# Kernel optimization log

Measured on AMD Instinct MI355X. Metric: run time of the kernel, lower is better.

The kernel has to match this reference:

```python
import jax, jax.numpy as jnp
import numpy as np

NUM_HEADS = 16

def setup_inputs() -> dict:
    key = jax.random.key(0)
    k1, k2, k3 = jax.random.split(key, 3)
    D = 1024
    return {
        "hidden_states": jax.random.normal(k1, (2, 2048, D), dtype=jnp.float32),
        "c_attn_w": jax.random.normal(k2, (D, 3 * D), dtype=jnp.float32) * 0.02,
        "c_attn_b": jnp.zeros((3 * D,), dtype=jnp.float32),
        "c_proj_w": jax.random.normal(k3, (D, D), dtype=jnp.float32) * 0.02,
        "c_proj_b": jnp.zeros((D,), dtype=jnp.float32),
    }

def reference(hidden_states, c_attn_w, c_attn_b, c_proj_w, c_proj_b):
    B, S, D = hidden_states.shape
    H = NUM_HEADS
    hd = D // H
    # Conv1D: x @ W + b, then split into q, k, v
    qkv = hidden_states @ c_attn_w + c_attn_b  # [B, S, 3D]
    q, k, v = jnp.split(qkv, 3, axis=-1)
    q = q.reshape(B, S, H, hd).transpose(0, 2, 1, 3)  # [B, H, S, hd]
    k = k.reshape(B, S, H, hd).transpose(0, 2, 1, 3)
    v = v.reshape(B, S, H, hd).transpose(0, 2, 1, 3)
    # scaled QK^T
    scores = jnp.einsum("bhqd,bhkd->bhqk", q, k) / jnp.asarray(hd ** 0.5, q.dtype)
    # causal mask (tril), masked positions set to dtype min per original code
    causal = jnp.tril(jnp.ones((S, S), dtype=bool))
    mask_value = jnp.finfo(scores.dtype).min
    scores = jnp.where(causal[None, None], scores, mask_value)
    attn = jax.nn.softmax(scores, axis=-1)
    out = jnp.einsum("bhqk,bhkd->bhqd", attn, v)  # [B, H, S, hd]
    out = out.transpose(0, 2, 1, 3).reshape(B, S, D)
    out = out @ c_proj_w + c_proj_b
    return out
```

## Files before the change

kernel.cpp:

```cpp
#include <hip/hip_runtime.h>
#include <hip/hip_bf16.h>
#include <math.h>

#define B_ 2
#define S_ 2048
#define D_ 1024
#define H_ 16
#define HD 64
#define M_ (B_ * S_)
#define N_QKV (3 * D_)

typedef short short8 __attribute__((ext_vector_type(8)));
typedef float floatx4 __attribute__((ext_vector_type(4)));

static __device__ __forceinline__ unsigned short f2bf(float x) {
    __hip_bfloat16 h = __float2bfloat16(x);
    unsigned short u;
    __builtin_memcpy(&u, &h, sizeof(u));
    return u;
}
static __device__ __forceinline__ float bf2f(unsigned short b) {
    union { unsigned u; float f; } v; v.u = ((unsigned)b) << 16;
    return v.f;
}
static __device__ __forceinline__ void split2(float x, unsigned short& h, unsigned short& l) {
    h = f2bf(x);
    l = f2bf(x - bf2f(h));
}

static __device__ __forceinline__ void dma16(const void* g, void* l) {
    __builtin_amdgcn_global_load_lds(
        (const __attribute__((address_space(1))) unsigned int*)g,
        (__attribute__((address_space(3))) unsigned int*)l,
        16, 0, 0);
}

__global__ __launch_bounds__(256) void prep_A(
    const float* __restrict__ X,
    unsigned short* __restrict__ Ahi, unsigned short* __restrict__ Alo)
{
    const size_t i = ((size_t)blockIdx.x * 256 + threadIdx.x) * 8;
    float4 a = *(const float4*)(X + i);
    float4 b = *(const float4*)(X + i + 4);
    float xs[8] = {a.x, a.y, a.z, a.w, b.x, b.y, b.z, b.w};
    short8 h, l;
#pragma unroll
    for (int e = 0; e < 8; e++) {
        unsigned short hh, ll;
        split2(xs[e], hh, ll);
        h[e] = (short)hh; l[e] = (short)ll;
    }
    *(short8*)&Ahi[i] = h;
    *(short8*)&Alo[i] = l;
}

__global__ __launch_bounds__(256) void prep_wT(
    const float* __restrict__ W, int N,
    unsigned short* __restrict__ Thi, unsigned short* __restrict__ Tlo)
{
    __shared__ float Ws[64][68];
    const int t  = threadIdx.x;
    const int n0 = blockIdx.x * 64, k0 = blockIdx.y * 64;
    {
        const int kl = t >> 4, nl = (t & 15) * 4;
        const float* src = W + (size_t)(k0 + kl) * N + n0 + nl;
#pragma unroll
        for (int g = 0; g < 4; g++)
            *(float4*)&Ws[kl + g * 16][nl] = *(const float4*)(src + (size_t)g * 16 * N);
    }
    __syncthreads();
    {
        const int nl = t >> 2, ks = (t & 3) * 16;
        short8 h0, h1, l0, l1;
#pragma unroll
        for (int j = 0; j < 8; j++) {
            unsigned short hh, ll;
            split2(Ws[ks + j][nl], hh, ll);
            h0[j] = (short)hh; l0[j] = (short)ll;
        }
#pragma unroll
        for (int j = 0; j < 8; j++) {
            unsigned short hh, ll;
            split2(Ws[ks + 8 + j][nl], hh, ll);
            h1[j] = (short)hh; l1[j] = (short)ll;
        }
        unsigned short* dh = Thi + (size_t)(n0 + nl) * D_ + k0 + ks;
        unsigned short* dl = Tlo + (size_t)(n0 + nl) * D_ + k0 + ks;
        *(short8*)dh = h0; *(short8*)(dh + 8) = h1;
        *(short8*)dl = l0; *(short8*)(dl + 8) = l1;
    }
}

__global__ __launch_bounds__(256) void gemm_qkv(
    const unsigned short* __restrict__ Ahi, const unsigned short* __restrict__ Alo,
    const unsigned short* __restrict__ BThi, const unsigned short* __restrict__ BTlo,
    const float* __restrict__ bias,
    unsigned short* __restrict__ Qhi, unsigned short* __restrict__ Qlo,
    unsigned short* __restrict__ Khi, unsigned short* __restrict__ Klo,
    unsigned short* __restrict__ vThi, unsigned short* __restrict__ vTlo)
{
    __shared__ unsigned short sAh[128 * 32], sAl[128 * 32];
    __shared__ unsigned short sBh[128 * 32], sBl[128 * 32];

    const int t    = threadIdx.x;
    const int m0   = blockIdx.y * 128, n0 = blockIdx.x * 128;
    const int lane = t & 63, wave = t >> 6;
    const int lm   = lane & 15, quad = lane >> 4;
    const int wm   = (wave >> 1) * 64, wn = (wave & 1) * 64;

    const int lrow = lane >> 2, lcol = (lane & 3) * 8;
    const unsigned short* gAh = Ahi + (size_t)(m0 + wave * 32 + lrow) * D_ + lcol;
    const unsigned short* gAl = Alo + (size_t)(m0 + wave * 32 + lrow) * D_ + lcol;
    const unsigned short* gBh = BThi + (size_t)(n0 + wave * 32 + lrow) * D_ + lcol;
    const unsigned short* gBl = BTlo + (size_t)(n0 + wave * 32 + lrow) * D_ + lcol;
    const int ldst = wave * 1024 + lane * 8;

    floatx4 acc[4][4];
#pragma unroll
    for (int i = 0; i < 4; i++)
#pragma unroll
        for (int j = 0; j < 4; j++)
#pragma unroll
            for (int r = 0; r < 4; r++) acc[i][j][r] = 0.f;

    for (int k0 = 0; k0 < D_; k0 += 32) {
        __syncthreads();
        dma16(gAh + k0, &sAh[ldst]);
        dma16(gAh + (size_t)16 * D_ + k0, &sAh[ldst + 512]);
        dma16(gAl + k0, &sAl[ldst]);
        dma16(gAl + (size_t)16 * D_ + k0, &sAl[ldst + 512]);
        dma16(gBh + k0, &sBh[ldst]);
        dma16(gBh + (size_t)16 * D_ + k0, &sBh[ldst + 512]);
        dma16(gBl + k0, &sBl[ldst]);
        dma16(gBl + (size_t)16 * D_ + k0, &sBl[ldst + 512]);
        __syncthreads();

        short8 bhf[4], blf[4];
#pragma unroll
        for (int nb = 0; nb < 4; nb++) {
            const int r = wn + nb * 16 + lm;
            bhf[nb] = *(const short8*)&sBh[r * 32 + quad * 8];
            blf[nb] = *(const short8*)&sBl[r * 32 + quad * 8];
        }
#pragma unroll
        for (int mb = 0; mb < 4; mb++) {
            const int r = wm + mb * 16 + lm;
            short8 ah = *(const short8*)&sAh[r * 32 + quad * 8];
            short8 al = *(const short8*)&sAl[r * 32 + quad * 8];
#pragma unroll
            for (int nb = 0; nb < 4; nb++) {
                acc[mb][nb] = __builtin_amdgcn_mfma_f32_16x16x32_bf16(ah, bhf[nb], acc[mb][nb], 0, 0, 0);
                acc[mb][nb] = __builtin_amdgcn_mfma_f32_16x16x32_bf16(al, bhf[nb], acc[mb][nb], 0, 0, 0);
                acc[mb][nb] = __builtin_amdgcn_mfma_f32_16x16x32_bf16(ah, blf[nb], acc[mb][nb], 0, 0, 0);
            }
        }
    }

    const int nmode = n0 >> 10;
    if (nmode == 0) {
#pragma unroll
        for (int nb = 0; nb < 4; nb++) {
            const int c = n0 + wn + nb * 16 + lm;
            const float bv = bias[c];
#pragma unroll
            for (int mb = 0; mb < 4; mb++) {
                const int rowb = m0 + wm + mb * 16 + quad * 4;
#pragma unroll
                for (int r = 0; r < 4; r++) {
                    unsigned short hh, ll;
                    split2((acc[mb][nb][r] + bv) * 0.125f, hh, ll);
                    Qhi[(size_t)(rowb + r) * D_ + c] = hh;
                    Qlo[(size_t)(rowb + r) * D_ + c] = ll;
                }
            }
        }
    } else if (nmode == 1) {
#pragma unroll
        for (int nb = 0; nb < 4; nb++) {
            const int c = n0 + wn + nb * 16 + lm;
            const float bv = bias[c];
            const int cq = c - 1024;
#pragma unroll
            for (int mb = 0; mb < 4; mb++) {
                const int rowb = m0 + wm + mb * 16 + quad * 4;
#pragma unroll
                for (int r = 0; r < 4; r++) {
                    unsigned short hh, ll;
                    split2(acc[mb][nb][r] + bv, hh, ll);
                    Khi[(size_t)(rowb + r) * D_ + cq] = hh;
                    Klo[(size_t)(rowb + r) * D_ + cq] = ll;
                }
            }
        }
    } else {
#pragma unroll
        for (int nb = 0; nb < 4; nb++) {
            const int c = n0 + wn + nb * 16 + lm;
            const float bv = bias[c];
            const int cq = c - 2048;
            const int hh_ = cq >> 6, dd = cq & 63;
#pragma unroll
            for (int mb = 0; mb < 4; mb++) {
                const int rowb = m0 + wm + mb * 16 + quad * 4;
                const int bb = rowb >> 11, ss = rowb & 2047;
                unsigned short hv[4], lv[4];
#pragma unroll
                for (int r = 0; r < 4; r++)
                    split2(acc[mb][nb][r] + bv, hv[r], lv[r]);
                const size_t idx = ((size_t)((bb * 16 + hh_) * 64 + dd)) * S_ + ss;
                *(uint2*)&vThi[idx] = make_uint2((unsigned)hv[0] | ((unsigned)hv[1] << 16),
                                                 (unsigned)hv[2] | ((unsigned)hv[3] << 16));
                *(uint2*)&vTlo[idx] = make_uint2((unsigned)lv[0] | ((unsigned)lv[1] << 16),
                                                 (unsigned)lv[2] | ((unsigned)lv[3] << 16));
            }
        }
    }
}

__global__ __launch_bounds__(256) void gemm_out(
    const unsigned short* __restrict__ Ahi, const unsigned short* __restrict__ Alo,
    const unsigned short* __restrict__ BThi, const unsigned short* __restrict__ BTlo,
    const float* __restrict__ bias, float* __restrict__ C)
{
    __shared__ unsigned short sAh[64 * 32], sAl[64 * 32];
    __shared__ unsigned short sBh[64 * 32], sBl[64 * 32];

    const int t   = threadIdx.x;
    const int lid = blockIdx.x;
    const int swz = (lid & 7) * 128 + (lid >> 3);
    const int bx  = swz & 15, by = swz >> 4;
    const int m0  = by * 64, n0 = bx * 64;
    const int lane = t & 63, wave = t >> 6;
    const int lm   = lane & 15, quad = lane >> 4;

    const int lrow = lane >> 2, lcol = (lane & 3) * 8;
    const unsigned short* gAh = Ahi + (size_t)(m0 + wave * 16 + lrow) * D_ + lcol;
    const unsigned short* gAl = Alo + (size_t)(m0 + wave * 16 + lrow) * D_ + lcol;
    const unsigned short* gBh = BThi + (size_t)(n0 + wave * 16 + lrow) * D_ + lcol;
    const unsigned short* gBl = BTlo + (size_t)(n0 + wave * 16 + lrow) * D_ + lcol;
    unsigned short* lAh = sAh + wave * 512 + lane * 8;
    unsigned short* lAl = sAl + wave * 512 + lane * 8;
    unsigned short* lBh = sBh + wave * 512 + lane * 8;
    unsigned short* lBl = sBl + wave * 512 + lane * 8;

    floatx4 acc[4];
#pragma unroll
    for (int j = 0; j < 4; j++)
#pragma unroll
        for (int r = 0; r < 4; r++) acc[j][r] = 0.f;

    for (int k0 = 0; k0 < D_; k0 += 32) {
        __syncthreads();
        dma16(gAh + k0, lAh);
        dma16(gAl + k0, lAl);
        dma16(gBh + k0, lBh);
        dma16(gBl + k0, lBl);
        __syncthreads();

        short8 ah = *(const short8*)&sAh[(wave * 16 + lm) * 32 + quad * 8];
        short8 al = *(const short8*)&sAl[(wave * 16 + lm) * 32 + quad * 8];
#pragma unroll
        for (int nb = 0; nb < 4; nb++) {
            short8 bh = *(const short8*)&sBh[(nb * 16 + lm) * 32 + quad * 8];
            short8 bl = *(const short8*)&sBl[(nb * 16 + lm) * 32 + quad * 8];
            acc[nb] = __builtin_amdgcn_mfma_f32_16x16x32_bf16(ah, bh, acc[nb], 0, 0, 0);
            acc[nb] = __builtin_amdgcn_mfma_f32_16x16x32_bf16(al, bh, acc[nb], 0, 0, 0);
            acc[nb] = __builtin_amdgcn_mfma_f32_16x16x32_bf16(ah, bl, acc[nb], 0, 0, 0);
        }
    }

#pragma unroll
    for (int nb = 0; nb < 4; nb++) {
        const int col = n0 + nb * 16 + lm;
        const float bv = bias[col];
#pragma unroll
        for (int r = 0; r < 4; r++) {
            const int row = m0 + wave * 16 + quad * 4 + r;
            C[(size_t)row * D_ + col] = acc[nb][r] + bv;
        }
    }
}

#define PSP 72

__global__ __launch_bounds__(256, 3) void flash_attn_mfma(
    unsigned short* QAhi, unsigned short* QAlo,
    const unsigned short* __restrict__ Khi, const unsigned short* __restrict__ Klo,
    const unsigned short* __restrict__ vThi, const unsigned short* __restrict__ vTlo)
{
    __shared__ unsigned short KhS[64 * 64], KlS[64 * 64];
    __shared__ unsigned short VhS[64 * 64], VlS[64 * 64];
    __shared__ unsigned short PhS[64 * PSP], PlS[64 * PSP];

    const int t    = threadIdx.x;
    const int pj   = blockIdx.x;
    const int bh   = blockIdx.y;
    const int b    = bh >> 4, h = bh & 15;
    const int lane = t & 63, w = t >> 6;
    const int lm   = lane & 15, quad = lane >> 4;

    const int r0  = t >> 3;
    const int seg = (t & 7) ^ (r0 & 7);
    const unsigned short* gKh = Khi + (size_t)(b * S_ + r0) * D_ + h * HD + 8 * seg;
    const unsigned short* gKl = Klo + (size_t)(b * S_ + r0) * D_ + h * HD + 8 * seg;
    const unsigned short* gVh = vThi + ((size_t)((b * 16 + h) * 64 + r0)) * S_ + 8 * seg;
    const unsigned short* gVl = vTlo + ((size_t)((b * 16 + h) * 64 + r0)) * S_ + 8 * seg;
    const int ld0 = t * 8;
    const int swzr = (lm & 7) << 3;

    for (int phse = 0; phse < 2; phse++) {
        const int qt = phse ? (31 - pj) : pj;
        const int q0 = qt * 64;
        const int ntiles = qt + 1;

        short8 qh[2], ql[2];
        {
            const size_t qoff = (size_t)(b * S_ + q0 + 16 * w + lm) * D_ + h * HD + quad * 8;
            qh[0] = *(const short8*)&QAhi[qoff];
            qh[1] = *(const short8*)&QAhi[qoff + 32];
            ql[0] = *(const short8*)&QAlo[qoff];
            ql[1] = *(const short8*)&QAlo[qoff + 32];
        }

        float lsum[4] = {0.f, 0.f, 0.f, 0.f};
        floatx4 o[4];
#pragma unroll
        for (int nb = 0; nb < 4; nb++)
#pragma unroll
            for (int r = 0; r < 4; r++) o[nb][r] = 0.f;

        for (int kt = 0; kt < ntiles; kt++) {
            __syncthreads();
            {
                const size_t ko = (size_t)(kt * 64) * D_;
                const int vo = kt * 64;
                dma16(gKh + ko,                    &KhS[ld0]);
                dma16(gKh + ko + (size_t)32 * D_,  &KhS[ld0 + 2048]);
                dma16(gKl + ko,                    &KlS[ld0]);
                dma16(gKl + ko + (size_t)32 * D_,  &KlS[ld0 + 2048]);
                dma16(gVh + vo,                    &VhS[ld0]);
                dma16(gVh + vo + (size_t)32 * S_,  &VhS[ld0 + 2048]);
                dma16(gVl + vo,                    &VlS[ld0]);
                dma16(gVl + vo + (size_t)32 * S_,  &VlS[ld0 + 2048]);
            }
            __syncthreads();

            floatx4 sa[4];
#pragma unroll
            for (int nb = 0; nb < 4; nb++)
#pragma unroll
                for (int r = 0; r < 4; r++) sa[nb][r] = 0.f;
            __builtin_amdgcn_s_setprio(1);
#pragma unroll
            for (int s = 0; s < 2; s++) {
#pragma unroll
                for (int nb = 0; nb < 4; nb++) {
                    const int ka = (nb * 16 + lm) * 64 + ((s * 32 + quad * 8) ^ swzr);
                    short8 kh = *(const short8*)&KhS[ka];
                    short8 kl = *(const short8*)&KlS[ka];
                    sa[nb] = __builtin_amdgcn_mfma_f32_16x16x32_bf16(qh[s], kh, sa[nb], 0, 0, 0);
                    sa[nb] = __builtin_amdgcn_mfma_f32_16x16x32_bf16(ql[s], kh, sa[nb], 0, 0, 0);
                    sa[nb] = __builtin_amdgcn_mfma_f32_16x16x32_bf16(qh[s], kl, sa[nb], 0, 0, 0);
                }
            }
            __builtin_amdgcn_s_setprio(0);

            const bool diag = (kt == qt);
            const int kbase = kt * 64;
#pragma unroll
            for (int r = 0; r < 4; r++) {
                const int qabs = q0 + 16 * w + 4 * quad + r;
                const int rloc = 16 * w + 4 * quad + r;
#pragma unroll
                for (int nb = 0; nb < 4; nb++) {
                    float p = __expf(sa[nb][r]);
                    if (diag && (kbase + 16 * nb + lm > qabs)) p = 0.f;
                    lsum[r] += p;
                    unsigned short hh, ll;
                    split2(p, hh, ll);
                    PhS[rloc * PSP + 16 * nb + lm] = hh;
                    PlS[rloc * PSP + 16 * nb + lm] = ll;
                }
            }

            __builtin_amdgcn_s_setprio(1);
#pragma unroll
            for (int ks = 0; ks < 2; ks++) {
                short8 pf = *(const short8*)&PhS[(16 * w + lm) * PSP + ks * 32 + quad * 8];
                short8 pg = *(const short8*)&PlS[(16 * w + lm) * PSP + ks * 32 + quad * 8];
#pragma unroll
                for (int nb = 0; nb < 4; nb++) {
                    const int va = (nb * 16 + lm) * 64 + ((ks * 32 + quad * 8) ^ swzr);
                    short8 vhf = *(const short8*)&VhS[va];
                    short8 vlf = *(const short8*)&VlS[va];
                    o[nb] = __builtin_amdgcn_mfma_f32_16x16x32_bf16(pf, vhf, o[nb], 0, 0, 0);
                    o[nb] = __builtin_amdgcn_mfma_f32_16x16x32_bf16(pg, vhf, o[nb], 0, 0, 0);
                    o[nb] = __builtin_amdgcn_mfma_f32_16x16x32_bf16(pf, vlf, o[nb], 0, 0, 0);
                }
            }
            __builtin_amdgcn_s_setprio(0);
        }

#pragma unroll
        for (int r = 0; r < 4; r++) {
            float l = lsum[r];
            l += __shfl_xor(l, 1);
            l += __shfl_xor(l, 2);
            l += __shfl_xor(l, 4);
            l += __shfl_xor(l, 8);
            const float inv = 1.f / l;
            const size_t rowoff =
                (size_t)(b * S_ + q0 + 16 * w + 4 * quad + r) * D_ + h * HD + lm;
#pragma unroll
            for (int nb = 0; nb < 4; nb++) {
                unsigned short hh, ll;
                split2(o[nb][r] * inv, hh, ll);
                QAhi[rowoff + 16 * nb] = hh;
                QAlo[rowoff + 16 * nb] = ll;
            }
        }
    }
}

extern "C" void kernel_launch(void* const* d_in, const int* in_sizes, int n_in,
                              void* d_out, int out_size, void* d_ws, size_t ws_size,
                              hipStream_t stream)
{
    const float* hs     = (const float*)d_in[0];
    const float* attn_w = (const float*)d_in[1];
    const float* attn_b = (const float*)d_in[2];
    const float* proj_w = (const float*)d_in[3];
    const float* proj_b = (const float*)d_in[4];
    float* outp = (float*)d_out;

    const size_t QE = (size_t)M_ * D_;
    const size_t WQ = (size_t)D_ * N_QKV;
    unsigned short* Qhi   = (unsigned short*)d_ws;
    unsigned short* Qlo   = Qhi + QE;
    unsigned short* Khi   = Qlo + QE;
    unsigned short* Klo   = Khi + QE;
    unsigned short* vThi  = Klo + QE;
    unsigned short* vTlo  = vThi + QE;
    unsigned short* WqThi = vTlo + QE;
    unsigned short* WqTlo = WqThi + WQ;
    unsigned short* WpThi = WqTlo + WQ;
    unsigned short* WpTlo = WpThi + (size_t)D_ * D_;
    unsigned short* Ahi   = WpTlo + (size_t)D_ * D_;
    unsigned short* Alo   = Ahi + QE;

    dim3 blk(256);
    prep_A<<<dim3(M_ * D_ / 2048), blk, 0, stream>>>(hs, Ahi, Alo);
    prep_wT<<<dim3(N_QKV / 64, D_ / 64), blk, 0, stream>>>(attn_w, N_QKV, WqThi, WqTlo);
    prep_wT<<<dim3(D_ / 64, D_ / 64), blk, 0, stream>>>(proj_w, D_, WpThi, WpTlo);
    gemm_qkv<<<dim3(N_QKV / 128, M_ / 128), blk, 0, stream>>>(
        Ahi, Alo, WqThi, WqTlo, attn_b, Qhi, Qlo, Khi, Klo, vThi, vTlo);
    flash_attn_mfma<<<dim3(16, B_ * H_), dim3(256), 0, stream>>>(
        Qhi, Qlo, Khi, Klo, vThi, vTlo);
    gemm_out<<<dim3(1024), blk, 0, stream>>>(
        Qhi, Qlo, WpThi, WpTlo, proj_b, outp);
}
```

Before: 307.2 us.

## Use 128x128 tiles with split-K in output projection GEMM

Rewrites the output projection GEMM to use 128x128 block tiles with each wave computing a 64x64 sub-tile, which increases register-level reuse of A and B fragments. The K dimension is split in two so the grid still has enough blocks. The second half writes partial sums into a scratch buffer that aliases the no-longer-needed K workspace, and a separate kernel adds them. The trade is an extra launch plus an extra read-modify-write of the output, in exchange for fewer shared-memory loads per MFMA.

```diff
diff --git a/kernel.cpp b/kernel.cpp
--- a/kernel.cpp
+++ b/kernel.cpp
@@ -220,65 +220,102 @@
 __global__ __launch_bounds__(256) void gemm_out(
     const unsigned short* __restrict__ Ahi, const unsigned short* __restrict__ Alo,
     const unsigned short* __restrict__ BThi, const unsigned short* __restrict__ BTlo,
-    const float* __restrict__ bias, float* __restrict__ C)
-{
-    __shared__ unsigned short sAh[64 * 32], sAl[64 * 32];
-    __shared__ unsigned short sBh[64 * 32], sBl[64 * 32];
-
-    const int t   = threadIdx.x;
-    const int lid = blockIdx.x;
-    const int swz = (lid & 7) * 128 + (lid >> 3);
-    const int bx  = swz & 15, by = swz >> 4;
-    const int m0  = by * 64, n0 = bx * 64;
+    const float* __restrict__ bias, float* __restrict__ C, float* __restrict__ P)
+{
+    __shared__ unsigned short sAh[128 * 32], sAl[128 * 32];
+    __shared__ unsigned short sBh[128 * 32], sBl[128 * 32];
+
+    const int t     = threadIdx.x;
+    const int m0    = blockIdx.y * 128, n0 = blockIdx.x * 128;
+    const int kbase = blockIdx.z * 512;
     const int lane = t & 63, wave = t >> 6;
     const int lm   = lane & 15, quad = lane >> 4;
+    const int wm   = (wave >> 1) * 64, wn = (wave & 1) * 64;
 
     const int lrow = lane >> 2, lcol = (lane & 3) * 8;
-    const unsigned short* gAh = Ahi + (size_t)(m0 + wave * 16 + lrow) * D_ + lcol;
-    const unsigned short* gAl = Alo + (size_t)(m0 + wave * 16 + lrow) * D_ + lcol;
-    const unsigned short* gBh = BThi + (size_t)(n0 + wave * 16 + lrow) * D_ + lcol;
-    const unsigned short* gBl = BTlo + (size_t)(n0 + wave * 16 + lrow) * D_ + lcol;
-    unsigned short* lAh = sAh + wave * 512 + lane * 8;
-    unsigned short* lAl = sAl + wave * 512 + lane * 8;
-    unsigned short* lBh = sBh + wave * 512 + lane * 8;
-    unsigned short* lBl = sBl + wave * 512 + lane * 8;
-
-    floatx4 acc[4];
-#pragma unroll
-    for (int j = 0; j < 4; j++)
-#pragma unroll
-        for (int r = 0; r < 4; r++) acc[j][r] = 0.f;
-
-    for (int k0 = 0; k0 < D_; k0 += 32) {
+    const unsigned short* gAh = Ahi + (size_t)(m0 + wave * 32 + lrow) * D_ + lcol + kbase;
+    const unsigned short* gAl = Alo + (size_t)(m0 + wave * 32 + lrow) * D_ + lcol + kbase;
+    const unsigned short* gBh = BThi + (size_t)(n0 + wave * 32 + lrow) * D_ + lcol + kbase;
+    const unsigned short* gBl = BTlo + (size_t)(n0 + wave * 32 + lrow) * D_ + lcol + kbase;
+    const int ldst = wave * 1024 + lane * 8;
+
+    floatx4 acc[4][4];
+#pragma unroll
+    for (int i = 0; i < 4; i++)
+#pragma unroll
+        for (int j = 0; j < 4; j++)
+#pragma unroll
+            for (int r = 0; r < 4; r++) acc[i][j][r] = 0.f;
+
+    for (int k0 = 0; k0 < 512; k0 += 32) {
         __syncthreads();
-        dma16(gAh + k0, lAh);
-        dma16(gAl + k0, lAl);
-        dma16(gBh + k0, lBh);
-        dma16(gBl + k0, lBl);
+        dma16(gAh + k0, &sAh[ldst]);
+        dma16(gAh + (size_t)16 * D_ + k0, &sAh[ldst + 512]);
+        dma16(gAl + k0, &sAl[ldst]);
+        dma16(gAl + (size_t)16 * D_ + k0, &sAl[ldst + 512]);
+        dma16(gBh + k0, &sBh[ldst]);
+        dma16(gBh + (size_t)16 * D_ + k0, &sBh[ldst + 512]);
+        dma16(gBl + k0, &sBl[ldst]);
+        dma16(gBl + (size_t)16 * D_ + k0, &sBl[ldst + 512]);
         __syncthreads();
 
-        short8 ah = *(const short8*)&sAh[(wave * 16 + lm) * 32 + quad * 8];
-        short8 al = *(const short8*)&sAl[(wave * 16 + lm) * 32 + quad * 8];
-#pragma unroll
-        for (int nb = 0; nb < 4; nb++) {
-            short8 bh = *(const short8*)&sBh[(nb * 16 + lm) * 32 + quad * 8];
-            short8 bl = *(const short8*)&sBl[(nb * 16 + lm) * 32 + quad * 8];
-            acc[nb] = __builtin_amdgcn_mfma_f32_16x16x32_bf16(ah, bh, acc[nb], 0, 0, 0);
-            acc[nb] = __builtin_amdgcn_mfma_f32_16x16x32_bf16(al, bh, acc[nb], 0, 0, 0);
-            acc[nb] = __builtin_amdgcn_mfma_f32_16x16x32_bf16(ah, bl, acc[nb], 0, 0, 0);
-        }
-    }
-
-#pragma unroll
-    for (int nb = 0; nb < 4; nb++) {
-        const int col = n0 + nb * 16 + lm;
-        const float bv = bias[col];
-#pragma unroll
-        for (int r = 0; r < 4; r++) {
-            const int row = m0 + wave * 16 + quad * 4 + r;
-            C[(size_t)row * D_ + col] = acc[nb][r] + bv;
-        }
-    }
+        short8 bhf[4], blf[4];
+#pragma unroll
+        for (int nb = 0; nb < 4; nb++) {
+            const int r = wn + nb * 16 + lm;
+            bhf[nb] = *(const short8*)&sBh[r * 32 + quad * 8];
+            blf[nb] = *(const short8*)&sBl[r * 32 + quad * 8];
+        }
+#pragma unroll
+        for (int mb = 0; mb < 4; mb++) {
+            const int r = wm + mb * 16 + lm;
+            short8 ah = *(const short8*)&sAh[r * 32 + quad * 8];
+            short8 al = *(const short8*)&sAl[r * 32 + quad * 8];
+#pragma unroll
+            for (int nb = 0; nb < 4; nb++) {
+                acc[mb][nb] = __builtin_amdgcn_mfma_f32_16x16x32_bf16(ah, bhf[nb], acc[mb][nb], 0, 0, 0);
+                acc[mb][nb] = __builtin_amdgcn_mfma_f32_16x16x32_bf16(al, bhf[nb], acc[mb][nb], 0, 0, 0);
+                acc[mb][nb] = __builtin_amdgcn_mfma_f32_16x16x32_bf16(ah, blf[nb], acc[mb][nb], 0, 0, 0);
+            }
+        }
+    }
+
+    if (blockIdx.z == 0) {
+#pragma unroll
+        for (int nb = 0; nb < 4; nb++) {
+            const int c = n0 + wn + nb * 16 + lm;
+            const float bv = bias[c];
+#pragma unroll
+            for (int mb = 0; mb < 4; mb++) {
+                const int rowb = m0 + wm + mb * 16 + quad * 4;
+#pragma unroll
+                for (int r = 0; r < 4; r++)
+                    C[(size_t)(rowb + r) * D_ + c] = acc[mb][nb][r] + bv;
+            }
+        }
+    } else {
+#pragma unroll
+        for (int nb = 0; nb < 4; nb++) {
+            const int c = n0 + wn + nb * 16 + lm;
+#pragma unroll
+            for (int mb = 0; mb < 4; mb++) {
+                const int rowb = m0 + wm + mb * 16 + quad * 4;
+#pragma unroll
+                for (int r = 0; r < 4; r++)
+                    P[(size_t)(rowb + r) * D_ + c] = acc[mb][nb][r];
+            }
+        }
+    }
+}
+
+__global__ __launch_bounds__(256) void add_partial(
+    float* __restrict__ C, const float* __restrict__ P)
+{
+    const size_t i = ((size_t)blockIdx.x * 256 + threadIdx.x) * 4;
+    float4 c = *(const float4*)(C + i);
+    float4 p = *(const float4*)(P + i);
+    c.x += p.x; c.y += p.y; c.z += p.z; c.w += p.w;
+    *(float4*)(C + i) = c;
 }
 
 #define PSP 72
@@ -448,6 +485,8 @@
     unsigned short* Ahi   = WpTlo + (size_t)D_ * D_;
     unsigned short* Alo   = Ahi + QE;
 
+    float* Pbuf = (float*)Khi;
+
     dim3 blk(256);
     prep_A<<<dim3(M_ * D_ / 2048), blk, 0, stream>>>(hs, Ahi, Alo);
     prep_wT<<<dim3(N_QKV / 64, D_ / 64), blk, 0, stream>>>(attn_w, N_QKV, WqThi, WqTlo);
@@ -456,6 +495,7 @@
         Ahi, Alo, WqThi, WqTlo, attn_b, Qhi, Qlo, Khi, Klo, vThi, vTlo);
     flash_attn_mfma<<<dim3(16, B_ * H_), dim3(256), 0, stream>>>(
         Qhi, Qlo, Khi, Klo, vThi, vTlo);
-    gemm_out<<<dim3(1024), blk, 0, stream>>>(
-        Qhi, Qlo, WpThi, WpTlo, proj_b, outp);
-}
+    gemm_out<<<dim3(D_ / 128, M_ / 128, 2), blk, 0, stream>>>(
+        Qhi, Qlo, WpThi, WpTlo, proj_b, outp, Pbuf);
+    add_partial<<<dim3(M_ * D_ / 1024), blk, 0, stream>>>(outp, Pbuf);
+}
```

Result: slower. 316.8 us (+3.1%).
